# Optimization experiments

Measured on AMD Instinct MI355X. Metric: run time of the kernel, lower is better.

The kernel has to match this reference:

```python
import jax, jax.numpy as jnp
import numpy as np

B_SZ, L, H, P = 16, 1024, 256, 256
DT_MIN, DT_MAX = 1e-3, 1e-1


def setup_inputs() -> dict:
    key = jax.random.key(0)
    ks = jax.random.split(key, 6)
    u = jax.random.normal(ks[0], (B_SZ, L, H), dtype=jnp.float32)
    # Stable diagonal init (stands in for HiPPO-LegS diag: negative real part,
    # spread imaginary parts) so exp(Lambda*Delta) has |.|<1 over long scans.
    Lambda_re = -0.5 * jnp.ones((P,), jnp.float32)
    Lambda_im = jnp.pi * jnp.arange(P, dtype=jnp.float32)
    Bp = jax.random.normal(ks[1], (P, H, 2), jnp.float32) / jnp.sqrt(2.0 * H)  # (P,H,2) real/imag
    Cp = jax.random.normal(ks[2], (H, P, 2), jnp.float32) / jnp.sqrt(2.0 * P)  # (H,P,2) real/imag
    D = jax.random.normal(ks[3], (H,), jnp.float32)
    log_step = (jax.random.uniform(ks[4], (P, 1), jnp.float32)
                * (jnp.log(DT_MAX) - jnp.log(DT_MIN)) + jnp.log(DT_MIN))
    return {"u": u, "Lambda_re": Lambda_re, "Lambda_im": Lambda_im,
            "B": Bp, "C": Cp, "D": D, "log_step": log_step}


def _binop(ei, ej):
    # S5 associative scan element: (A, Bu); compose linear recurrences.
    ai, bi = ei
    aj, bj = ej
    return aj * ai, aj * bi + bj


def reference(u, Lambda_re, Lambda_im, B, C, D, log_step):
    # clip_eigs=False, step_rescale=1.0, conj_sym=True, discretization='zoh'
    Lambda = Lambda_re + 1j * Lambda_im                     # (P,) complex
    B_tilde = B[..., 0] + 1j * B[..., 1]                    # (P,H) complex
    C_tilde = C[..., 0] + 1j * C[..., 1]                    # (H,P) complex
    Delta = jnp.exp(log_step[:, 0])                         # (P,)
    # ZOH discretization
    Lambda_bar = jnp.exp(Lambda * Delta)                    # (P,)
    B_bar = ((Lambda_bar - 1.0) / Lambda)[:, None] * B_tilde  # (P,H)
    # Input projection: (B, L, P) complex
    Bu = jnp.einsum('ph,blh->blp', B_bar, u.astype(B_bar.dtype))
    Lam = jnp.broadcast_to(Lambda_bar, Bu.shape)            # (B, L, P)
    # Parallel associative scan over time axis
    _, xs = jax.lax.associative_scan(_binop, (Lam, Bu), axis=1)  # states (B,L,P)
    # Output projection; conj_sym -> 2 * real part
    ys = 2.0 * jnp.einsum('hp,blp->blh', C_tilde, xs).real  # (B,L,H)
    return ys + D * u                                       # feedthrough
```

## Files before the change

kernel.cpp:

```cpp
#include <hip/hip_runtime.h>
#include <hip/hip_bf16.h>
#include <math.h>

#define BB     16
#define LSEQ   1024
#define HH     256
#define PP     256
#define MROWS  (BB*LSEQ)
#define LC     32
#define NC     (LSEQ/LC)
#define NCHUNK (BB*NC)

#define OFF_W1T  0u
#define OFF_W2T  262144u
#define OFF_PW   524288u
#define OFF_CEND 655360u
#define OFF_XS   2752512u

typedef __attribute__((ext_vector_type(8))) short short8;
typedef __attribute__((ext_vector_type(4))) float floatx4;

__device__ __forceinline__ float bf2f(unsigned hs) {
    union { unsigned u; float f; } v; v.u = hs << 16; return v.f;
}
__device__ __forceinline__ unsigned short f2bs(float f) {
    __hip_bfloat16 h = __float2bfloat16(f);
    union { __hip_bfloat16 h; unsigned short s; } v; v.h = h; return v.s;
}
__device__ __forceinline__ unsigned packbf(float r, float i) {
    return (unsigned)f2bs(r) | ((unsigned)f2bs(i) << 16);
}
__device__ __forceinline__ void async16(const void* g, void* l) {
    __builtin_amdgcn_global_load_lds(
        (const __attribute__((address_space(1))) unsigned*)g,
        (__attribute__((address_space(3))) unsigned*)l, 16, 0, 0);
}
__device__ __forceinline__ float2 lam_pow(float lr, float li, float dtt) {
    float m = expf(lr * dtt);
    return make_float2(m * cosf(li * dtt), m * sinf(li * dtt));
}

__global__ void k_prep(const float* __restrict__ Bm, const float* __restrict__ Cm,
                       const float* __restrict__ Lr, const float* __restrict__ Li,
                       const float* __restrict__ ls, char* __restrict__ ws) {
    int blk = blockIdx.x, t = threadIdx.x;
    if (blk < 256) {
        int p = blk, h = t;
        float lr = Lr[p], li = Li[p];
        float dt = expf(ls[p]);
        float2 lam = lam_pow(lr, li, dt);
        float den = lr * lr + li * li;
        float nr = lam.x - 1.0f, ni = lam.y;
        float cr = (nr * lr + ni * li) / den;
        float ci = (ni * lr - nr * li) / den;
        float br = Bm[(p * HH + h) * 2 + 0];
        float bi = Bm[(p * HH + h) * 2 + 1];
        unsigned short* w1 = (unsigned short*)(ws + OFF_W1T);
        w1[(2 * p) * 256 + h]     = f2bs(cr * br - ci * bi);
        w1[(2 * p + 1) * 256 + h] = f2bs(cr * bi + ci * br);
        if (t <= 32)
            ((float2*)(ws + OFF_PW))[t * 256 + p] = lam_pow(lr, li, dt * (float)t);
    } else {
        int h = blk - 256, p = t;
        float c_r = Cm[(h * PP + p) * 2 + 0];
        float c_i = Cm[(h * PP + p) * 2 + 1];
        ((unsigned*)(ws + OFF_W2T))[h * 256 + p] = packbf(2.0f * c_r, -2.0f * c_i);
    }
}

#define XSTR2 268
__global__ __launch_bounds__(512, 6) void k_g1scan(
        const float* __restrict__ u, const float* __restrict__ Lr,
        const float* __restrict__ Li, const float* __restrict__ ls,
        char* __restrict__ ws) {
    __shared__ char smem[36864];
    char* Asb = smem;
    char* Bsb = smem + 4096;
    unsigned short* X = (unsigned short*)smem;
    unsigned* X32 = (unsigned*)smem;
    const unsigned short* W1 = (const unsigned short*)(ws + OFF_W1T);
    const int tid = threadIdx.x, bx = blockIdx.x;
    const int nh = bx & 1, bc = bx >> 1;
    const int m0 = bc * LC, n0 = nh * 256;
    const int wave = tid >> 6, lane = tid & 63;
    const int q = lane >> 4, rr = lane & 15;
    const int c4 = lane & 3, r4 = lane >> 2;

    floatx4 acc[2][2];
    #pragma unroll
    for (int i = 0; i < 2; ++i)
        #pragma unroll
        for (int j = 0; j < 2; ++j) acc[i][j] = (floatx4)0.0f;

    const int arow = tid >> 4, acol4 = (tid & 15) * 4;
    for (int k0 = 0; k0 < 256; k0 += 64) {
        __syncthreads();
        {
            float4 v = *(const float4*)(u + (size_t)(m0 + arow) * 256 + k0 + acol4);
            *(uint2*)(Asb + (acol4 >> 5) * 2048 + arow * 64 + (acol4 & 31) * 2) =
                make_uint2(packbf(v.x, v.y), packbf(v.z, v.w));
        }
        #pragma unroll
        for (int t = 0; t < 4; ++t) {
            int idx = t * 8 + wave;
            int pan = idx & 1, rowg = idx >> 1;
            int row = rowg * 16 + r4;
            async16(W1 + (size_t)(n0 + row) * 256 + k0 + pan * 32 + c4 * 8,
                    Bsb + pan * 16384 + row * 64 + c4 * 16);
        }
        __syncthreads();
        #pragma unroll
        for (int ks = 0; ks < 2; ++ks) {
            short8 a0 = *(const short8*)(Asb + ks * 2048 + rr * 64 + q * 16);
            short8 a1 = *(const short8*)(Asb + ks * 2048 + (16 + rr) * 64 + q * 16);
            #pragma unroll
            for (int j = 0; j < 2; ++j) {
                short8 b = *(const short8*)(Bsb + ks * 16384 +
                                            (wave * 32 + j * 16 + rr) * 64 + q * 16);
                acc[0][j] = __builtin_amdgcn_mfma_f32_16x16x32_bf16(a0, b, acc[0][j], 0, 0, 0);
                acc[1][j] = __builtin_amdgcn_mfma_f32_16x16x32_bf16(a1, b, acc[1][j], 0, 0, 0);
            }
        }
    }
    __syncthreads();
    #pragma unroll
    for (int i = 0; i < 2; ++i)
        #pragma unroll
        for (int j = 0; j < 2; ++j)
            #pragma unroll
            for (int r0 = 0; r0 < 4; ++r0)
                X[(i * 16 + q * 4 + r0) * XSTR2 + wave * 32 + j * 16 + rr] =
                    f2bs(acc[i][j][r0]);
    __syncthreads();

    if (tid < 128) {
        const int pq = tid;
        const int gp = nh * 128 + pq;
        const float2 lam = lam_pow(Lr[gp], Li[gp], expf(ls[gp]));
        unsigned* xs32 = (unsigned*)(ws + OFF_XS);
        float xr = 0.0f, xi = 0.0f;
        for (int j = 0; j < LC; ++j) {
            unsigned cv = X32[j * (XSTR2 / 2) + pq];
            float br = bf2f(cv & 0xffffu), bi = bf2f(cv >> 16);
            float nr = fmaf(lam.x, xr, fmaf(-lam.y, xi, br));
            float ni = fmaf(lam.x, xi, fmaf(lam.y, xr, bi));
            xr = nr; xi = ni;
            xs32[(size_t)(m0 + j) * 256 + gp] = packbf(xr, xi);
        }
        ((float2*)(ws + OFF_CEND))[(size_t)bc * 256 + gp] = make_float2(xr, xi);
    }
}

__global__ __launch_bounds__(256, 4) void k_gemm2fix(
        const char* __restrict__ ws_c, const float* __restrict__ D,
        const float* __restrict__ u, float* __restrict__ out,
        const float* __restrict__ Lr, const float* __restrict__ Li,
        const float* __restrict__ ls) {
    __shared__ char Asb[8192];
    __shared__ char Bsb[16384];
    __shared__ float2 carrs[2][256];
    const unsigned short* W2 = (const unsigned short*)(ws_c + OFF_W2T);
    const unsigned* xs32 = (const unsigned*)(ws_c + OFF_XS);
    const float2* pw = (const float2*)(ws_c + OFF_PW);
    const float2* cend = (const float2*)(ws_c + OFF_CEND);

    const int tid = threadIdx.x;
    const int wave = tid >> 6, lane = tid & 63;
    const int q = lane >> 4, rr = lane & 15;
    const int c4 = lane & 3, r4 = lane >> 2;
    const int wm = wave & 1, wn = wave >> 1;
    const int m0 = blockIdx.y * 64, n0 = blockIdx.x * 128;

    {
        const int cbase = m0 >> 5;
        const int b = cbase >> 5, c = cbase & 31;
        const int p = tid;
        const float2 g = lam_pow(Lr[p], Li[p], expf(ls[p]) * (float)LC);
        float sr = 0.0f, si = 0.0f;
        float gpr = 1.0f, gpi = 0.0f;
        for (int k = 0; k < c; ++k) {
            float2 e = cend[(size_t)(b * NC + (c - 1 - k)) * 256 + p];
            sr = fmaf(gpr, e.x, fmaf(-gpi, e.y, sr));
            si = fmaf(gpr, e.y, fmaf(gpi, e.x, si));
            float t = gpr * g.x - gpi * g.y;
            gpi = gpr * g.y + gpi * g.x; gpr = t;
        }
        carrs[0][p] = make_float2(sr, si);
        float2 e = cend[(size_t)cbase * 256 + p];
        carrs[1][p] = make_float2(fmaf(g.x, sr, fmaf(-g.y, si, e.x)),
                                  fmaf(g.x, si, fmaf(g.y, sr, e.y)));
    }

    floatx4 acc[2][4];
    #pragma unroll
    for (int i = 0; i < 2; ++i)
        #pragma unroll
        for (int j = 0; j < 4; ++j) acc[i][j] = (floatx4)0.0f;

    const int row = tid >> 2, qd = tid & 3;
    const int grow = m0 + row;
    const int jj = (grow & (LC - 1)) + 1;
    const int half = row >> 5;

    for (int k0 = 0; k0 < 512; k0 += 64) {
        __syncthreads();
        {
            int p0 = (k0 >> 1) + qd * 8;
            uint4 xa = *(const uint4*)(xs32 + (size_t)grow * 256 + p0);
            uint4 xb = *(const uint4*)(xs32 + (size_t)grow * 256 + p0 + 4);
            unsigned xv[8] = {xa.x, xa.y, xa.z, xa.w, xb.x, xb.y, xb.z, xb.w};
            const float2* pwp = pw + (size_t)jj * 256 + p0;
            const float2* cap = &carrs[half][p0];
            unsigned o[8];
            #pragma unroll
            for (int e = 0; e < 8; ++e) {
                float2 pwv = pwp[e];
                float2 cav = cap[e];
                float fr = pwv.x * cav.x - pwv.y * cav.y;
                float fi = pwv.x * cav.y + pwv.y * cav.x;
                o[e] = packbf(bf2f(xv[e] & 0xffffu) + fr, bf2f(xv[e] >> 16) + fi);
            }
            char* dst = Asb + (qd >> 1) * 4096 + row * 64 + (qd & 1) * 32;
            *(uint4*)dst        = make_uint4(o[0], o[1], o[2], o[3]);
            *(uint4*)(dst + 16) = make_uint4(o[4], o[5], o[6], o[7]);
        }
        #pragma unroll
        for (int t = 0; t < 4; ++t) {
            int idx = t * 4 + wave;
            int pan = idx & 1, rowg = idx >> 1;
            int rw = rowg * 16 + r4;
            async16(W2 + (size_t)(n0 + rw) * 512 + k0 + pan * 32 + c4 * 8,
                    Bsb + pan * 8192 + rw * 64 + c4 * 16);
        }
        __syncthreads();
        #pragma unroll
        for (int ks = 0; ks < 2; ++ks) {
            short8 a[2], bfr[4];
            #pragma unroll
            for (int i = 0; i < 2; ++i)
                a[i] = *(const short8*)(Asb + ks * 4096 +
                                        (wm * 32 + i * 16 + rr) * 64 + q * 16);
            #pragma unroll
            for (int j = 0; j < 4; ++j)
                bfr[j] = *(const short8*)(Bsb + ks * 8192 +
                                          ((wn * 64 + j * 16 + rr)) * 64 + q * 16);
            #pragma unroll
            for (int i = 0; i < 2; ++i)
                #pragma unroll
                for (int j = 0; j < 4; ++j)
                    acc[i][j] = __builtin_amdgcn_mfma_f32_16x16x32_bf16(a[i], bfr[j], acc[i][j], 0, 0, 0);
        }
    }

    #pragma unroll
    for (int i = 0; i < 2; ++i) {
        int mbase = m0 + wm * 32 + i * 16 + q * 4;
        #pragma unroll
        for (int j = 0; j < 4; ++j) {
            int col = n0 + wn * 64 + j * 16 + rr;
            #pragma unroll
            for (int r0 = 0; r0 < 4; ++r0) {
                int rw = mbase + r0;
                size_t gi = (size_t)rw * 256 + col;
                out[gi] = acc[i][j][r0] + D[col] * u[gi];
            }
        }
    }
}

extern "C" void kernel_launch(void* const* d_in, const int* in_sizes, int n_in,
                              void* d_out, int out_size, void* d_ws, size_t ws_size,
                              hipStream_t stream) {
    const float* u  = (const float*)d_in[0];
    const float* Lr = (const float*)d_in[1];
    const float* Li = (const float*)d_in[2];
    const float* Bm = (const float*)d_in[3];
    const float* Cm = (const float*)d_in[4];
    const float* D  = (const float*)d_in[5];
    const float* ls = (const float*)d_in[6];
    float* out = (float*)d_out;
    char* ws = (char*)d_ws;

    k_prep<<<512, 256, 0, stream>>>(Bm, Cm, Lr, Li, ls, ws);
    k_g1scan<<<1024, 512, 0, stream>>>(u, Lr, Li, ls, ws);
    k_gemm2fix<<<dim3(2, MROWS / 64), 256, 0, stream>>>(ws, D, u, out, Lr, Li, ls);
}
```

Measured before the change: 113.5 us.

## Precompute chunk carries in a sequential carry kernel and widen GEMM tiles

```diff
diff --git a/kernel.cpp b/kernel.cpp
--- a/kernel.cpp
+++ b/kernel.cpp
@@ -15,6 +15,7 @@
 #define OFF_W2T  262144u
 #define OFF_PW   524288u
 #define OFF_CEND 655360u
+#define OFF_CARR 1703936u
 #define OFF_XS   2752512u
 
 typedef __attribute__((ext_vector_type(8))) short short8;
@@ -68,29 +69,29 @@
     }
 }
 
-#define XSTR2 268
-__global__ __launch_bounds__(512, 6) void k_g1scan(
+#define XSTRD 514
+#define XSTRS 1028
+__global__ __launch_bounds__(512, 4) void k_g1scan(
         const float* __restrict__ u, const float* __restrict__ Lr,
         const float* __restrict__ Li, const float* __restrict__ ls,
         char* __restrict__ ws) {
-    __shared__ char smem[36864];
+    extern __shared__ char smem[];
     char* Asb = smem;
     char* Bsb = smem + 4096;
     unsigned short* X = (unsigned short*)smem;
     unsigned* X32 = (unsigned*)smem;
     const unsigned short* W1 = (const unsigned short*)(ws + OFF_W1T);
-    const int tid = threadIdx.x, bx = blockIdx.x;
-    const int nh = bx & 1, bc = bx >> 1;
-    const int m0 = bc * LC, n0 = nh * 256;
+    const int tid = threadIdx.x, bc = blockIdx.x;
+    const int m0 = bc * LC;
     const int wave = tid >> 6, lane = tid & 63;
     const int q = lane >> 4, rr = lane & 15;
     const int c4 = lane & 3, r4 = lane >> 2;
 
-    floatx4 acc[2][2];
+    floatx4 acc[2][4];
     #pragma unroll
     for (int i = 0; i < 2; ++i)
         #pragma unroll
-        for (int j = 0; j < 2; ++j) acc[i][j] = (floatx4)0.0f;
+        for (int j = 0; j < 4; ++j) acc[i][j] = (floatx4)0.0f;
 
     const int arow = tid >> 4, acol4 = (tid & 15) * 4;
     for (int k0 = 0; k0 < 256; k0 += 64) {
@@ -101,12 +102,12 @@
                 make_uint2(packbf(v.x, v.y), packbf(v.z, v.w));
         }
         #pragma unroll
-        for (int t = 0; t < 4; ++t) {
+        for (int t = 0; t < 8; ++t) {
             int idx = t * 8 + wave;
             int pan = idx & 1, rowg = idx >> 1;
             int row = rowg * 16 + r4;
-            async16(W1 + (size_t)(n0 + row) * 256 + k0 + pan * 32 + c4 * 8,
-                    Bsb + pan * 16384 + row * 64 + c4 * 16);
+            async16(W1 + (size_t)row * 256 + k0 + pan * 32 + c4 * 8,
+                    Bsb + pan * 32768 + row * 64 + c4 * 16);
         }
         __syncthreads();
         #pragma unroll
@@ -114,9 +115,9 @@
             short8 a0 = *(const short8*)(Asb + ks * 2048 + rr * 64 + q * 16);
             short8 a1 = *(const short8*)(Asb + ks * 2048 + (16 + rr) * 64 + q * 16);
             #pragma unroll
-            for (int j = 0; j < 2; ++j) {
-                short8 b = *(const short8*)(Bsb + ks * 16384 +
-                                            (wave * 32 + j * 16 + rr) * 64 + q * 16);
+            for (int j = 0; j < 4; ++j) {
+                short8 b = *(const short8*)(Bsb + ks * 32768 +
+                                            (wave * 64 + j * 16 + rr) * 64 + q * 16);
                 acc[0][j] = __builtin_amdgcn_mfma_f32_16x16x32_bf16(a0, b, acc[0][j], 0, 0, 0);
                 acc[1][j] = __builtin_amdgcn_mfma_f32_16x16x32_bf16(a1, b, acc[1][j], 0, 0, 0);
             }
@@ -126,70 +127,67 @@
     #pragma unroll
     for (int i = 0; i < 2; ++i)
         #pragma unroll
-        for (int j = 0; j < 2; ++j)
+        for (int j = 0; j < 4; ++j)
             #pragma unroll
             for (int r0 = 0; r0 < 4; ++r0)
-                X[(i * 16 + q * 4 + r0) * XSTR2 + wave * 32 + j * 16 + rr] =
+                X[(i * 16 + q * 4 + r0) * XSTRS + wave * 64 + j * 16 + rr] =
                     f2bs(acc[i][j][r0]);
     __syncthreads();
 
-    if (tid < 128) {
+    if (tid < 256) {
         const int pq = tid;
-        const int gp = nh * 128 + pq;
-        const float2 lam = lam_pow(Lr[gp], Li[gp], expf(ls[gp]));
+        const float2 lam = lam_pow(Lr[pq], Li[pq], expf(ls[pq]));
         unsigned* xs32 = (unsigned*)(ws + OFF_XS);
         float xr = 0.0f, xi = 0.0f;
+        #pragma unroll
         for (int j = 0; j < LC; ++j) {
-            unsigned cv = X32[j * (XSTR2 / 2) + pq];
+            unsigned cv = X32[j * XSTRD + pq];
             float br = bf2f(cv & 0xffffu), bi = bf2f(cv >> 16);
             float nr = fmaf(lam.x, xr, fmaf(-lam.y, xi, br));
             float ni = fmaf(lam.x, xi, fmaf(lam.y, xr, bi));
             xr = nr; xi = ni;
-            xs32[(size_t)(m0 + j) * 256 + gp] = packbf(xr, xi);
-        }
-        ((float2*)(ws + OFF_CEND))[(size_t)bc * 256 + gp] = make_float2(xr, xi);
+            xs32[(size_t)(m0 + j) * 256 + pq] = packbf(xr, xi);
+        }
+        ((float2*)(ws + OFF_CEND))[(size_t)bc * 256 + pq] = make_float2(xr, xi);
+    }
+}
+
+__global__ void k_carry(const float* __restrict__ Lr, const float* __restrict__ Li,
+                        const float* __restrict__ ls, char* __restrict__ ws) {
+    const int b = blockIdx.x, p = threadIdx.x;
+    const float2* cend = (const float2*)(ws + OFF_CEND);
+    float2* carr = (float2*)(ws + OFF_CARR);
+    const float2 g = lam_pow(Lr[p], Li[p], expf(ls[p]) * (float)LC);
+    float sr = 0.0f, si = 0.0f;
+    #pragma unroll
+    for (int c = 0; c < NC; ++c) {
+        size_t idx = (size_t)(b * NC + c) * 256 + p;
+        carr[idx] = make_float2(sr, si);
+        float2 e = cend[idx];
+        float nr = fmaf(g.x, sr, fmaf(-g.y, si, e.x));
+        float ni = fmaf(g.x, si, fmaf(g.y, sr, e.y));
+        sr = nr; si = ni;
     }
 }
 
 __global__ __launch_bounds__(256, 4) void k_gemm2fix(
         const char* __restrict__ ws_c, const float* __restrict__ D,
-        const float* __restrict__ u, float* __restrict__ out,
-        const float* __restrict__ Lr, const float* __restrict__ Li,
-        const float* __restrict__ ls) {
-    __shared__ char Asb[8192];
-    __shared__ char Bsb[16384];
-    __shared__ float2 carrs[2][256];
+        const float* __restrict__ u, float* __restrict__ out) {
+    __shared__ char Asb[4096];
+    __shared__ char Bsb[32768];
+    __shared__ float2 carrs[256];
     const unsigned short* W2 = (const unsigned short*)(ws_c + OFF_W2T);
     const unsigned* xs32 = (const unsigned*)(ws_c + OFF_XS);
     const float2* pw = (const float2*)(ws_c + OFF_PW);
-    const float2* cend = (const float2*)(ws_c + OFF_CEND);
+    const float2* carr = (const float2*)(ws_c + OFF_CARR);
 
     const int tid = threadIdx.x;
     const int wave = tid >> 6, lane = tid & 63;
     const int q = lane >> 4, rr = lane & 15;
     const int c4 = lane & 3, r4 = lane >> 2;
-    const int wm = wave & 1, wn = wave >> 1;
-    const int m0 = blockIdx.y * 64, n0 = blockIdx.x * 128;
-
-    {
-        const int cbase = m0 >> 5;
-        const int b = cbase >> 5, c = cbase & 31;
-        const int p = tid;
-        const float2 g = lam_pow(Lr[p], Li[p], expf(ls[p]) * (float)LC);
-        float sr = 0.0f, si = 0.0f;
-        float gpr = 1.0f, gpi = 0.0f;
-        for (int k = 0; k < c; ++k) {
-            float2 e = cend[(size_t)(b * NC + (c - 1 - k)) * 256 + p];
-            sr = fmaf(gpr, e.x, fmaf(-gpi, e.y, sr));
-            si = fmaf(gpr, e.y, fmaf(gpi, e.x, si));
-            float t = gpr * g.x - gpi * g.y;
-            gpi = gpr * g.y + gpi * g.x; gpr = t;
-        }
-        carrs[0][p] = make_float2(sr, si);
-        float2 e = cend[(size_t)cbase * 256 + p];
-        carrs[1][p] = make_float2(fmaf(g.x, sr, fmaf(-g.y, si, e.x)),
-                                  fmaf(g.x, si, fmaf(g.y, sr, e.y)));
-    }
+    const int m0 = blockIdx.x * LC;
+
+    carrs[tid] = carr[(size_t)blockIdx.x * 256 + tid];
 
     floatx4 acc[2][4];
     #pragma unroll
@@ -197,40 +195,36 @@
         #pragma unroll
         for (int j = 0; j < 4; ++j) acc[i][j] = (floatx4)0.0f;
 
-    const int row = tid >> 2, qd = tid & 3;
+    const int row = tid >> 3, qd = tid & 7;
     const int grow = m0 + row;
     const int jj = (grow & (LC - 1)) + 1;
-    const int half = row >> 5;
 
     for (int k0 = 0; k0 < 512; k0 += 64) {
         __syncthreads();
         {
-            int p0 = (k0 >> 1) + qd * 8;
+            int p0 = (k0 >> 1) + qd * 4;
             uint4 xa = *(const uint4*)(xs32 + (size_t)grow * 256 + p0);
-            uint4 xb = *(const uint4*)(xs32 + (size_t)grow * 256 + p0 + 4);
-            unsigned xv[8] = {xa.x, xa.y, xa.z, xa.w, xb.x, xb.y, xb.z, xb.w};
+            unsigned xv[4] = {xa.x, xa.y, xa.z, xa.w};
             const float2* pwp = pw + (size_t)jj * 256 + p0;
-            const float2* cap = &carrs[half][p0];
-            unsigned o[8];
-            #pragma unroll
-            for (int e = 0; e < 8; ++e) {
+            unsigned o[4];
+            #pragma unroll
+            for (int e = 0; e < 4; ++e) {
                 float2 pwv = pwp[e];
-                float2 cav = cap[e];
+                float2 cav = carrs[p0 + e];
                 float fr = pwv.x * cav.x - pwv.y * cav.y;
                 float fi = pwv.x * cav.y + pwv.y * cav.x;
                 o[e] = packbf(bf2f(xv[e] & 0xffffu) + fr, bf2f(xv[e] >> 16) + fi);
             }
-            char* dst = Asb + (qd >> 1) * 4096 + row * 64 + (qd & 1) * 32;
-            *(uint4*)dst        = make_uint4(o[0], o[1], o[2], o[3]);
-            *(uint4*)(dst + 16) = make_uint4(o[4], o[5], o[6], o[7]);
-        }
-        #pragma unroll
-        for (int t = 0; t < 4; ++t) {
+            char* dst = Asb + (qd >> 2) * 2048 + row * 64 + (qd & 3) * 16;
+            *(uint4*)dst = make_uint4(o[0], o[1], o[2], o[3]);
+        }
+        #pragma unroll
+        for (int t = 0; t < 8; ++t) {
             int idx = t * 4 + wave;
             int pan = idx & 1, rowg = idx >> 1;
             int rw = rowg * 16 + r4;
-            async16(W2 + (size_t)(n0 + rw) * 512 + k0 + pan * 32 + c4 * 8,
-                    Bsb + pan * 8192 + rw * 64 + c4 * 16);
+            async16(W2 + (size_t)rw * 512 + k0 + pan * 32 + c4 * 8,
+                    Bsb + pan * 16384 + rw * 64 + c4 * 16);
         }
         __syncthreads();
         #pragma unroll
@@ -238,12 +232,11 @@
             short8 a[2], bfr[4];
             #pragma unroll
             for (int i = 0; i < 2; ++i)
-                a[i] = *(const short8*)(Asb + ks * 4096 +
-                                        (wm * 32 + i * 16 + rr) * 64 + q * 16);
+                a[i] = *(const short8*)(Asb + ks * 2048 + (i * 16 + rr) * 64 + q * 16);
             #pragma unroll
             for (int j = 0; j < 4; ++j)
-                bfr[j] = *(const short8*)(Bsb + ks * 8192 +
-                                          ((wn * 64 + j * 16 + rr)) * 64 + q * 16);
+                bfr[j] = *(const short8*)(Bsb + ks * 16384 +
+                                          (wave * 64 + j * 16 + rr) * 64 + q * 16);
             #pragma unroll
             for (int i = 0; i < 2; ++i)
                 #pragma unroll
@@ -254,10 +247,10 @@
 
     #pragma unroll
     for (int i = 0; i < 2; ++i) {
-        int mbase = m0 + wm * 32 + i * 16 + q * 4;
+        int mbase = m0 + i * 16 + q * 4;
         #pragma unroll
         for (int j = 0; j < 4; ++j) {
-            int col = n0 + wn * 64 + j * 16 + rr;
+            int col = wave * 64 + j * 16 + rr;
             #pragma unroll
             for (int r0 = 0; r0 < 4; ++r0) {
                 int rw = mbase + r0;
@@ -282,6 +275,7 @@
     char* ws = (char*)d_ws;
 
     k_prep<<<512, 256, 0, stream>>>(Bm, Cm, Lr, Li, ls, ws);
-    k_g1scan<<<1024, 512, 0, stream>>>(u, Lr, Li, ls, ws);
-    k_gemm2fix<<<dim3(2, MROWS / 64), 256, 0, stream>>>(ws, D, u, out, Lr, Li, ls);
-}
+    k_g1scan<<<NCHUNK, 512, 69632, stream>>>(u, Lr, Li, ls, ws);
+    k_carry<<<BB, 256, 0, stream>>>(Lr, Li, ls, ws);
+    k_gemm2fix<<<NCHUNK, 256, 0, stream>>>(ws, D, u, out);
+}
```

Result: no change. 113.3 us (-0.2%).
